# Kernel tuning notes

Hardware: AMD Instinct MI355X
Metric: run time of the kernel (lower is better)

The kernel has to match this reference:

```python
import jax, jax.numpy as jnp
import numpy as np

LN_EPS = 1e-5
LOCAL_SIZE = 256
N_HEAD, D_HEAD = 16, 64


def layer_norm_c(x):
    # layer norm over channel dim (axis=1), no affine params (matches F.layer_norm(x.T,(d,)).T)
    m = jnp.mean(x, axis=1, keepdims=True)
    v = jnp.var(x, axis=1, keepdims=True)
    return (x - m) / jnp.sqrt(v + LN_EPS)


def rel_shift(x):
    # x: [b, n, q, k] -> Transformer-XL relative shift
    b, n, q, k = x.shape
    x = jnp.pad(x, ((0, 0), (0, 0), (0, 0), (1, 0)))
    return x.reshape(b, n, k + 1, q)[:, :, 1:].reshape(b, n, q, k)


def setup_inputs() -> dict:
    key = jax.random.key(0)
    ks = jax.random.split(key, 14)
    bsz, d_model, qlen, mlen = 4, 1024, 512, 512
    klen = qlen + mlen
    d_inner = 4096
    s = lambda k, shape, sc=0.05: jax.random.normal(k, shape, dtype=jnp.float32) * sc
    return {
        "z1ss": jax.random.normal(ks[0], (bsz, d_model, qlen), dtype=jnp.float32),
        "uss": jax.random.normal(ks[1], (bsz, 3 * d_model, klen), dtype=jnp.float32) * 0.1,
        "z0": jax.random.normal(ks[2], (bsz, d_model, mlen), dtype=jnp.float32),
        "pos_emb": jax.random.normal(ks[3], (1, d_model, klen), dtype=jnp.float32),
        "qkv_w": s(ks[4], (3 * d_model, d_model)),
        "r_w": s(ks[5], (d_model, d_model)),
        "r_w_bias": s(ks[6], (N_HEAD, D_HEAD)),
        "r_r_bias": s(ks[7], (N_HEAD, D_HEAD)),
        "o_w": s(ks[8], (d_model, d_model)),
        "o_b": s(ks[9], (d_model,)),
        "ff1_w": s(ks[10], (d_inner, d_model)),
        "ff1_b": s(ks[11], (d_inner,)),
        "ff2_w": s(ks[12], (d_model, d_inner)),
        "ff2_b": s(ks[13], (d_model,)),
    }


def reference(z1ss, uss, z0, pos_emb, qkv_w, r_w, r_w_bias, r_r_bias, o_w, o_b,
              ff1_w, ff1_b, ff2_w, ff2_b):
    bsz, d_model, qlen = z1ss.shape
    mlen = z0.shape[2]
    n_head, d_head = N_HEAD, D_HEAD
    scale = 1.0 / d_head ** 0.5

    # ---- self-attention (post-lnorm path) ----
    cat = jnp.concatenate([z0, z1ss], axis=-1)              # [b, d, klen]
    klen = cat.shape[2]
    w_heads = jnp.einsum('od,bdk->bok', qkv_w, cat) + uss   # [b, 3d, klen]
    r_head_k = jnp.einsum('od,dk->ok', r_w, pos_emb[0])     # [d, rlen]
    rlen = r_head_k.shape[1]

    w_head_q, w_head_k, w_head_v = jnp.split(w_heads, 3, axis=1)
    w_head_q = w_head_q[:, :, -qlen:]
    w_head_q = w_head_q.reshape(bsz, n_head, d_head, qlen)
    w_head_k = w_head_k.reshape(bsz, n_head, d_head, klen)
    w_head_v = w_head_v.reshape(bsz, n_head, d_head, klen)
    r_head_k = r_head_k.reshape(n_head, d_head, rlen)

    rw_q = w_head_q + r_w_bias[:, :, None]                  # [b,n,d,q]
    AC = jnp.einsum('bndi,bndj->bnij', rw_q, w_head_k)      # [b,n,q,k]
    rr_q = w_head_q + r_r_bias[:, :, None]
    BD = rel_shift(jnp.einsum('bndi,ndj->bnij', rr_q, r_head_k))
    attn_score = (AC + BD) * scale

    local_size = LOCAL_SIZE if LOCAL_SIZE else 1000
    i = jnp.arange(qlen)[:, None]
    j = jnp.arange(klen)[None, :]
    mask = (j > i + mlen) | (j <= i + mlen - local_size)    # causal + local window
    attn_score = jnp.where(mask[None, None], -jnp.inf, attn_score)

    attn_prob = jax.nn.softmax(attn_score, axis=-1)
    attn_vec = jnp.einsum('bnij,bndj->bndi', attn_prob, w_head_v)
    attn_vec = attn_vec.reshape(bsz, n_head * d_head, qlen)
    attn_out = jnp.einsum('od,bdq->boq', o_w, attn_vec) + o_b[None, :, None]
    x = layer_norm_c(attn_out + z1ss)                       # post-lnorm

    # ---- position-wise FF (weight-shared, post-lnorm) ----
    h = jax.nn.relu(jnp.einsum('id,bdq->biq', ff1_w, x) + ff1_b[None, :, None])
    out2 = jnp.einsum('di,biq->bdq', ff2_w, h) + ff2_b[None, :, None]
    return layer_norm_c(out2 + x)
```

## Files before the change

kernel.cpp:

```cpp
#include <hip/hip_runtime.h>
#include <hip/hip_bf16.h>

typedef unsigned short u16;
typedef __attribute__((ext_vector_type(8))) short s8v;
typedef __attribute__((ext_vector_type(4))) short s4v;
typedef __attribute__((ext_vector_type(4))) float f4v;

__device__ __forceinline__ float s2f(u16 s) {
    unsigned int u = ((unsigned int)s) << 16;
    return __builtin_bit_cast(float, u);
}
__device__ __forceinline__ u16 f2s(float f) {
    __hip_bfloat16 h = __float2bfloat16(f);
    return __builtin_bit_cast(u16, h);
}

__device__ __forceinline__ void gl2lds16(const u16* g, u16* l) {
    __builtin_amdgcn_global_load_lds((const __attribute__((address_space(1))) void*)g,
                                     (__attribute__((address_space(3))) void*)l, 16, 0, 0);
}

#define BSZ 4
#define DM 1024
#define QLEN 512
#define MLEN 512
#define KLEN 1024
#define DI 4096
#define NH 16
#define DH 64
#define WIN 256

__global__ __launch_bounds__(256) void conv_w5(
    const float* __restrict__ s0, const float* __restrict__ s1,
    const float* __restrict__ s2, const float* __restrict__ s3,
    const float* __restrict__ s4,
    u16* __restrict__ d0, u16* __restrict__ d1, u16* __restrict__ d2,
    u16* __restrict__ d3, u16* __restrict__ d4)
{
    const int e0 = 786432, e1 = e0 + 262144, e2 = e1 + 262144,
              e3 = e2 + 1048576, e4 = e3 + 1048576;
    int i = blockIdx.x * 256 + threadIdx.x;
    const float* s; u16* d; int off;
    if (i < e0)      { s = s0; d = d0; off = i; }
    else if (i < e1) { s = s1; d = d1; off = i - e0; }
    else if (i < e2) { s = s2; d = d2; off = i - e1; }
    else if (i < e3) { s = s3; d = d3; off = i - e2; }
    else if (i < e4) { s = s4; d = d4; off = i - e3; }
    else return;
    f4v v = *(const f4v*)&s[(size_t)off * 4];
    s4v o;
#pragma unroll
    for (int k = 0; k < 4; ++k) o[k] = (short)f2s(v[k]);
    *(s4v*)&d[(size_t)off * 4] = o;
}

__global__ __launch_bounds__(256) void trans_f2b(
    const float* __restrict__ src, long sS, int ldS, int colOff,
    u16* __restrict__ dst, long sD, int ldD, int rowOff)
{
    __shared__ float tile[32][33];
    int b = blockIdx.z;
    int t0 = blockIdx.x * 32, f0 = blockIdx.y * 32;
    int tx = threadIdx.x, ty = threadIdx.y;
#pragma unroll
    for (int p = 0; p < 4; ++p)
        tile[ty + 8 * p][tx] = src[(size_t)b * sS + (size_t)(f0 + ty + 8 * p) * ldS + colOff + t0 + tx];
    __syncthreads();
#pragma unroll
    for (int p = 0; p < 4; ++p)
        dst[(size_t)b * sD + (size_t)(rowOff + t0 + ty + 8 * p) * ldD + f0 + tx] = f2s(tile[tx][ty + 8 * p]);
}

__global__ __launch_bounds__(256) void uss_add(
    const float* __restrict__ uss, u16* __restrict__ whT, u16* __restrict__ vT)
{
    __shared__ float tile[32][33];
    int b = blockIdx.z;
    int t0 = blockIdx.x * 32, fy = blockIdx.y;
    int tx = threadIdx.x, ty = threadIdx.y;
    if (fy < 32 && t0 < 512) return;
    const float* S = uss + (size_t)b * 3072 * 1024;
    if (fy < 64) {
        int f0 = fy * 32;
        u16* D = whT + (size_t)b * 1024 * 3072;
#pragma unroll
        for (int p = 0; p < 4; ++p)
            tile[ty + 8 * p][tx] = S[(size_t)(f0 + ty + 8 * p) * 1024 + t0 + tx];
        __syncthreads();
#pragma unroll
        for (int p = 0; p < 4; ++p) {
            size_t o = (size_t)(t0 + ty + 8 * p) * 3072 + f0 + tx;
            D[o] = f2s(s2f(D[o]) + tile[tx][ty + 8 * p]);
        }
    } else {
        int d0 = (fy - 64) * 32;
#pragma unroll
        for (int p = 0; p < 4; ++p) {
            int d = d0 + ty + 8 * p;
            size_t ui = ((size_t)2048 + d) * 1024 + t0 + tx;
            size_t vi = (size_t)d * 4096 + (size_t)b * KLEN + t0 + tx;
            vT[vi] = f2s(s2f(vT[vi]) + S[ui]);
        }
    }
}

__global__ __launch_bounds__(256) void trans_b2f(
    const u16* __restrict__ src, long sS, int ldS,
    float* __restrict__ dst, long sD, int ldD)
{
    __shared__ float tile[32][33];
    int b = blockIdx.z;
    int t0 = blockIdx.x * 32, f0 = blockIdx.y * 32;
    int tx = threadIdx.x, ty = threadIdx.y;
#pragma unroll
    for (int p = 0; p < 4; ++p)
        tile[ty + 8 * p][tx] = s2f(src[(size_t)b * sS + (size_t)(f0 + ty + 8 * p) * ldS + t0 + tx]);
    __syncthreads();
#pragma unroll
    for (int p = 0; p < 4; ++p)
        dst[(size_t)b * sD + (size_t)(t0 + ty + 8 * p) * ldD + f0 + tx] = tile[tx][ty + 8 * p];
}

template<int BN, int SPLIT>
__global__ __launch_bounds__(256) void gemm_bt(
    const u16* __restrict__ A,
    const u16* __restrict__ B,
    u16* __restrict__ C,
    float* __restrict__ fOut,
    int M, int K,
    const float* __restrict__ bias,
    int relu,
    int qskip,
    long pstride,
    u16* __restrict__ vTout)
{
    constexpr int BM = 128, BK = 64;
    constexpr int MI = (BN == 128) ? 4 : 2;
    constexpr int NI = 4;
    const int n0 = blockIdx.x * BN, m0 = blockIdx.y * BM;
    if (qskip && m0 + BM <= 1024 && (n0 & 1023) < 512) return;
    const int Ks = K / SPLIT;
    const int kbeg = blockIdx.z * Ks;
    __shared__ __align__(16) u16 As[BM * BK];
    __shared__ __align__(16) u16 Bs[BN * BK];
    const int tid = threadIdx.x, lane = tid & 63, wv = tid >> 6;
    const int l15 = lane & 15, quad = lane >> 4;
    const int wm = (BN == 128) ? (wv >> 1) * 64 : wv * 32;
    const int wn = (BN == 128) ? (wv & 1) * 64 : 0;
    f4v acc[MI][NI] = {};
    for (int kk = kbeg; kk < kbeg + Ks; kk += BK) {
        __syncthreads();
#pragma unroll
        for (int p = 0; p < (BM * 8) / 256; ++p) {
            int c = p * 256 + tid, r = c >> 3, q = c & 7, qs = q ^ (r & 7);
            gl2lds16(&A[(size_t)(m0 + r) * K + kk + qs * 8], &As[c * 8]);
        }
#pragma unroll
        for (int p = 0; p < (BN * 8) / 256; ++p) {
            int c = p * 256 + tid, r = c >> 3, q = c & 7, qs = q ^ (r & 7);
            gl2lds16(&B[(size_t)(n0 + r) * K + kk + qs * 8], &Bs[c * 8]);
        }
        __syncthreads();
#pragma unroll
        for (int k0 = 0; k0 < BK; k0 += 32) {
            s8v af[MI], bf[NI];
#pragma unroll
            for (int mi = 0; mi < MI; ++mi) {
                int r = wm + mi * 16 + l15;
                af[mi] = *(const s8v*)&As[r * BK + ((((k0 >> 3) + quad) ^ (r & 7)) << 3)];
            }
#pragma unroll
            for (int ni = 0; ni < NI; ++ni) {
                int r = wn + ni * 16 + l15;
                bf[ni] = *(const s8v*)&Bs[r * BK + ((((k0 >> 3) + quad) ^ (r & 7)) << 3)];
            }
#pragma unroll
            for (int mi = 0; mi < MI; ++mi)
#pragma unroll
                for (int ni = 0; ni < NI; ++ni)
                    acc[mi][ni] = __builtin_amdgcn_mfma_f32_16x16x32_bf16(af[mi], bf[ni], acc[mi][ni], 0, 0, 0);
        }
    }
    if (SPLIT > 1) {
        float* base = fOut + (long)blockIdx.z * pstride;
#pragma unroll
        for (int mi = 0; mi < MI; ++mi) {
            int m = m0 + wm + mi * 16 + quad * 4;
#pragma unroll
            for (int ni = 0; ni < NI; ++ni) {
                int n = n0 + wn + ni * 16 + l15;
                *(f4v*)&base[(size_t)n * M + m] = acc[mi][ni];
            }
        }
    } else if (vTout && m0 >= 2048) {
#pragma unroll
        for (int mi = 0; mi < MI; ++mi) {
            int m = m0 + wm + mi * 16 + quad * 4;
#pragma unroll
            for (int ni = 0; ni < NI; ++ni) {
                int n = n0 + wn + ni * 16 + l15;
#pragma unroll
                for (int r2 = 0; r2 < 4; ++r2)
                    vTout[(size_t)(m + r2 - 2048) * 4096 + n] = f2s(acc[mi][ni][r2]);
            }
        }
    } else {
#pragma unroll
        for (int mi = 0; mi < MI; ++mi) {
            int m = m0 + wm + mi * 16 + quad * 4;
            float bv[4] = {0.f, 0.f, 0.f, 0.f};
            if (bias) {
#pragma unroll
                for (int r2 = 0; r2 < 4; ++r2) bv[r2] = bias[m + r2];
            }
#pragma unroll
            for (int ni = 0; ni < NI; ++ni) {
                int n = n0 + wn + ni * 16 + l15;
                float o[4];
#pragma unroll
                for (int r2 = 0; r2 < 4; ++r2) o[r2] = acc[mi][ni][r2] + bv[r2];
                if (relu) {
#pragma unroll
                    for (int r2 = 0; r2 < 4; ++r2) o[r2] = fmaxf(o[r2], 0.f);
                }
                s4v st;
#pragma unroll
                for (int r2 = 0; r2 < 4; ++r2) st[r2] = (short)f2s(o[r2]);
                *(s4v*)&C[(size_t)n * M + m] = st;
            }
        }
    }
}

#define QT 32
#define SROW 260
__global__ __launch_bounds__(256, 4) void attn_mfma(
    const u16* __restrict__ WHT,
    const u16* __restrict__ VT,
    const u16* __restrict__ RT,
    const float* __restrict__ rwb, const float* __restrict__ rrb,
    u16* __restrict__ avT)
{
    __shared__ __align__(16) float sS[QT * SROW];

    const int qt = blockIdx.x, n = blockIdx.y, b = blockIdx.z;
    const int i0 = qt * QT, j0 = i0 + WIN + 1;
    const int tid = threadIdx.x, lane = tid & 63, wv = tid >> 6;
    const int l15 = lane & 15, quad = lane >> 4;
    const u16* W = WHT + (size_t)b * KLEN * (3 * DM);

    s8v qac[2][2], qbd[2][2];
#pragma unroll
    for (int h = 0; h < 2; ++h) {
        int qrow = MLEN + i0 + 16 * h + l15;
#pragma unroll
        for (int kc = 0; kc < 2; ++kc) {
            int col = n * DH + kc * 32 + quad * 8;
            s8v qv = *(const s8v*)&W[(size_t)qrow * (3 * DM) + col];
            s8v a, c;
#pragma unroll
            for (int e = 0; e < 8; ++e) {
                float qf = s2f((u16)qv[e]);
                a[e] = (short)f2s(qf + rwb[col + e]);
                c[e] = (short)f2s(qf + rrb[col + e]);
            }
            qac[h][kc] = a; qbd[h][kc] = c;
        }
    }

    for (int ci = wv; ci < 18; ci += 4) {
        int j = j0 + ci * 16 + l15; if (j > KLEN - 1) j = KLEN - 1;
        const u16* Kr = &W[(size_t)j * (3 * DM) + DM + n * DH + quad * 8];
        s8v k0 = *(const s8v*)Kr, k1 = *(const s8v*)(Kr + 32);
#pragma unroll
        for (int h = 0; h < 2; ++h) {
            f4v acc = {};
            acc = __builtin_amdgcn_mfma_f32_16x16x32_bf16(qac[h][0], k0, acc, 0, 0, 0);
            acc = __builtin_amdgcn_mfma_f32_16x16x32_bf16(qac[h][1], k1, acc, 0, 0, 0);
#pragma unroll
            for (int r2 = 0; r2 < 4; ++r2) {
                int qi = 16 * h + quad * 4 + r2;
                int t = ci * 16 + l15 - qi;
                if ((unsigned)t < 256u) sS[qi * SROW + t] = acc[r2];
            }
        }
    }
    __syncthreads();

#pragma unroll
    for (int cc = 0; cc < 4; ++cc) {
        int ci = wv + cc * 4;
        const u16* Rr = &RT[(size_t)(ci * 16 + l15) * DM + n * DH + quad * 8];
        s8v r0 = *(const s8v*)Rr, r1 = *(const s8v*)(Rr + 32);
#pragma unroll
        for (int h = 0; h < 2; ++h) {
            f4v acc = {};
            acc = __builtin_amdgcn_mfma_f32_16x16x32_bf16(qbd[h][0], r0, acc, 0, 0, 0);
            acc = __builtin_amdgcn_mfma_f32_16x16x32_bf16(qbd[h][1], r1, acc, 0, 0, 0);
#pragma unroll
            for (int r2 = 0; r2 < 4; ++r2) {
                int qi = 16 * h + quad * 4 + r2;
                sS[qi * SROW + ci * 16 + l15] += acc[r2];
            }
        }
    }
    __syncthreads();

    {
        int g = tid >> 4, l = tid & 15;
#pragma unroll
        for (int h = 0; h < 2; ++h) {
            int r = g + 16 * h;
            float vals[16], mx = -1e30f;
#pragma unroll
            for (int k = 0; k < 16; ++k) {
                float s = sS[r * SROW + l + 16 * k] * 0.125f;
                vals[k] = s; mx = fmaxf(mx, s);
            }
            asm volatile("" ::: "memory");
#pragma unroll
            for (int d = 1; d < 16; d <<= 1) mx = fmaxf(mx, __shfl_xor(mx, d, 16));
            float sum = 0.f;
#pragma unroll
            for (int k = 0; k < 16; ++k) { vals[k] = __expf(vals[k] - mx); sum += vals[k]; }
#pragma unroll
            for (int d = 1; d < 16; d <<= 1) sum += __shfl_xor(sum, d, 16);
            float inv = 1.f / sum;
            u16* sPr = (u16*)&sS[r * SROW];
#pragma unroll
            for (int k = 0; k < 16; ++k) sPr[r + 1 + l + 16 * k] = f2s(vals[k] * inv);
            if (l <= r) sPr[l] = 0;
            if (l + 16 <= r) sPr[l + 16] = 0;
            int p = r + 257 + l;
            if (p < 288) sPr[p] = 0;
            p += 16;
            if (p < 288) sPr[p] = 0;
        }
    }
    __syncthreads();

    const u16* sPu = (const u16*)sS;
    const size_t vbase = (size_t)(n * DH + wv * 16 + l15) * 4096
                       + (size_t)b * KLEN + (j0 - 1) + quad * 8;
    f4v o0 = {}, o1 = {};
#pragma unroll
    for (int kc = 0; kc < 9; ++kc) {
        s8v bb = *(const s8v*)&VT[vbase + kc * 32];
        s8v a0 = *(const s8v*)&sPu[(size_t)l15 * (2 * SROW) + kc * 32 + quad * 8];
        s8v a1 = *(const s8v*)&sPu[(size_t)(16 + l15) * (2 * SROW) + kc * 32 + quad * 8];
        o0 = __builtin_amdgcn_mfma_f32_16x16x32_bf16(a0, bb, o0, 0, 0, 0);
        o1 = __builtin_amdgcn_mfma_f32_16x16x32_bf16(a1, bb, o1, 0, 0, 0);
    }
#pragma unroll
    for (int r2 = 0; r2 < 4; ++r2) {
        int qi = quad * 4 + r2;
        avT[((size_t)b * QLEN + i0 + qi) * DM + n * DH + wv * 16 + l15] = f2s(o0[r2]);
        avT[((size_t)b * QLEN + i0 + 16 + qi) * DM + n * DH + wv * 16 + l15] = f2s(o1[r2]);
    }
}

__global__ __launch_bounds__(256) void ln_f(
    const float* __restrict__ P, long pstride, int nparts,
    const float* __restrict__ bias,
    const u16* __restrict__ res, int resMode, u16* __restrict__ out)
{
    int n = blockIdx.x, tid = threadIdx.x;
    int lane = tid & 63, wv = tid >> 6;
    int f = tid * 4;
    int rrow = resMode ? (((n >> 9) * 2 + 1) * 512 + (n & 511)) : n;
    f4v pv = *(const f4v*)&P[(size_t)n * DM + f];
    for (int p = 1; p < nparts; ++p) {
        const float* Pp = P + (long)p * pstride;
        pv += *(const f4v*)&Pp[(size_t)n * DM + f];
    }
    s4v rv = *(const s4v*)&res[(size_t)rrow * DM + f];
    f4v bv = *(const f4v*)&bias[f];
    float v[4];
#pragma unroll
    for (int k = 0; k < 4; ++k) v[k] = pv[k] + bv[k] + s2f((u16)rv[k]);
    float s = v[0] + v[1] + v[2] + v[3];
    float ss = v[0] * v[0] + v[1] * v[1] + v[2] * v[2] + v[3] * v[3];
#pragma unroll
    for (int d = 1; d < 64; d <<= 1) {
        s += __shfl_xor(s, d, 64);
        ss += __shfl_xor(ss, d, 64);
    }
    __shared__ float ps[4], pss[4];
    if (lane == 0) { ps[wv] = s; pss[wv] = ss; }
    __syncthreads();
    float S = ps[0] + ps[1] + ps[2] + ps[3];
    float SS = pss[0] + pss[1] + pss[2] + pss[3];
    float m = S * (1.f / DM);
    float var = SS * (1.f / DM) - m * m;
    float inv = rsqrtf(fmaxf(var, 0.f) + 1e-5f);
    s4v st;
#pragma unroll
    for (int k = 0; k < 4; ++k) st[k] = (short)f2s((v[k] - m) * inv);
    *(s4v*)&out[(size_t)n * DM + f] = st;
}

extern "C" void kernel_launch(void* const* d_in, const int* in_sizes, int n_in,
                              void* d_out, int out_size, void* d_ws, size_t ws_size,
                              hipStream_t stream) {
    const float* z1ss  = (const float*)d_in[0];
    const float* uss   = (const float*)d_in[1];
    const float* z0    = (const float*)d_in[2];
    const float* pos   = (const float*)d_in[3];
    const float* qkv_w = (const float*)d_in[4];
    const float* r_w   = (const float*)d_in[5];
    const float* rwb   = (const float*)d_in[6];
    const float* rrb   = (const float*)d_in[7];
    const float* o_w   = (const float*)d_in[8];
    const float* o_b   = (const float*)d_in[9];
    const float* ff1_w = (const float*)d_in[10];
    const float* ff1_b = (const float*)d_in[11];
    const float* ff2_w = (const float*)d_in[12];
    const float* ff2_b = (const float*)d_in[13];

    u16* ws = (u16*)d_ws;
    u16* wQ   = ws;
    u16* wR   = ws + 3145728;
    u16* wO   = ws + 4194304;
    u16* wF1  = ws + 5242880;
    u16* wF2  = ws + 9437184;
    u16* catT = ws + 13631488;
    u16* whT  = ws + 17825792;
    u16* posT = ws + 30408704;
    u16* rT   = ws + 30670848;
    u16* avT  = ws + 30932992;
    u16* xT   = ws + 33030144;
    float* pref = (float*)(ws + 35127296);
    u16* hT   = whT;
    u16* outT = catT;

    u16* vT = (u16*)pref;

    float* part1 = (float*)d_ws;
    long pstr = part1 - pref;

    dim3 tblk(32, 8);

    conv_w5<<<13312, 256, 0, stream>>>(qkv_w, r_w, o_w, ff1_w, ff2_w,
                                       wQ, wR, wO, wF1, wF2);

    trans_f2b<<<dim3(16, 32, BSZ), tblk, 0, stream>>>(z0, (long)DM * MLEN, MLEN, 0,
                                                      catT, (long)KLEN * DM, DM, 0);
    trans_f2b<<<dim3(16, 32, BSZ), tblk, 0, stream>>>(z1ss, (long)DM * QLEN, QLEN, 0,
                                                      catT, (long)KLEN * DM, DM, MLEN);
    trans_f2b<<<dim3(8, 32, 1), tblk, 0, stream>>>(pos, 0, KLEN, KLEN - WIN,
                                                   posT, 0, DM, 0);

    gemm_bt<64, 1><<<dim3(64, 24, 1), 256, 0, stream>>>(
        wQ, catT, whT, nullptr, 3 * DM, DM, nullptr, 0, 1, 0, vT);

    uss_add<<<dim3(32, 96, BSZ), tblk, 0, stream>>>(uss, whT, vT);

    gemm_bt<64, 1><<<dim3(4, 8, 1), 256, 0, stream>>>(
        wR, posT, rT, nullptr, DM, DM, nullptr, 0, 0, 0, nullptr);

    attn_mfma<<<dim3(QLEN / QT, NH, BSZ), 256, 0, stream>>>(whT, vT, rT, rwb, rrb, avT);

    gemm_bt<64, 2><<<dim3(32, 8, 2), 256, 0, stream>>>(
        wO, avT, nullptr, pref, DM, DM, nullptr, 0, 0, pstr, nullptr);

    ln_f<<<2048, 256, 0, stream>>>(pref, pstr, 2, o_b, catT, 1, xT);

    gemm_bt<64, 1><<<dim3(32, 32, 1), 256, 0, stream>>>(
        wF1, xT, hT, nullptr, DI, DM, ff1_b, 1, 0, 0, nullptr);

    gemm_bt<64, 2><<<dim3(32, 8, 2), 256, 0, stream>>>(
        wF2, hT, nullptr, pref, DM, DI, nullptr, 0, 0, pstr, nullptr);

    ln_f<<<2048, 256, 0, stream>>>(pref, pstr, 2, ff2_b, xT, 0, outT);

    trans_b2f<<<dim3(32, 16, BSZ), tblk, 0, stream>>>(outT, (long)QLEN * DM, DM,
                                                      (float*)d_out, (long)DM * QLEN, QLEN);
}
```

Measured before the change: 337.5 us.

## Merge prep kernels into one launch and double attention query tile to 64

Merges the weight conversion kernel and the three transpose kernels into a single prep launch, so three launches and their inter-kernel gaps go away. The attention kernel now handles 64 query rows per block instead of 32. Each K/R/V fragment load is reused across four 16-row MFMA groups, and the window overhead per query shrinks, in exchange for half as many blocks, a larger LDS score buffer and lower occupancy (launch bounds 2).

```diff
diff --git a/kernel.cpp b/kernel.cpp
--- a/kernel.cpp
+++ b/kernel.cpp
@@ -30,38 +30,56 @@
 #define DH 64
 #define WIN 256
 
-__global__ __launch_bounds__(256) void conv_w5(
-    const float* __restrict__ s0, const float* __restrict__ s1,
-    const float* __restrict__ s2, const float* __restrict__ s3,
-    const float* __restrict__ s4,
-    u16* __restrict__ d0, u16* __restrict__ d1, u16* __restrict__ d2,
-    u16* __restrict__ d3, u16* __restrict__ d4)
-{
-    const int e0 = 786432, e1 = e0 + 262144, e2 = e1 + 262144,
-              e3 = e2 + 1048576, e4 = e3 + 1048576;
-    int i = blockIdx.x * 256 + threadIdx.x;
-    const float* s; u16* d; int off;
-    if (i < e0)      { s = s0; d = d0; off = i; }
-    else if (i < e1) { s = s1; d = d1; off = i - e0; }
-    else if (i < e2) { s = s2; d = d2; off = i - e1; }
-    else if (i < e3) { s = s3; d = d3; off = i - e2; }
-    else if (i < e4) { s = s4; d = d4; off = i - e3; }
-    else return;
-    f4v v = *(const f4v*)&s[(size_t)off * 4];
-    s4v o;
-#pragma unroll
-    for (int k = 0; k < 4; ++k) o[k] = (short)f2s(v[k]);
-    *(s4v*)&d[(size_t)off * 4] = o;
-}
-
-__global__ __launch_bounds__(256) void trans_f2b(
-    const float* __restrict__ src, long sS, int ldS, int colOff,
-    u16* __restrict__ dst, long sD, int ldD, int rowOff)
-{
+#define CONV_BLKS 13312
+#define Z0_BLKS 2048
+#define Z1_BLKS 2048
+#define POS_BLKS 256
+__global__ __launch_bounds__(256) void prep(
+    const float* __restrict__ qkv_w, const float* __restrict__ r_w,
+    const float* __restrict__ o_w, const float* __restrict__ ff1_w,
+    const float* __restrict__ ff2_w,
+    u16* __restrict__ wQ, u16* __restrict__ wR, u16* __restrict__ wO,
+    u16* __restrict__ wF1, u16* __restrict__ wF2,
+    const float* __restrict__ z0, const float* __restrict__ z1ss,
+    const float* __restrict__ pos,
+    u16* __restrict__ catT, u16* __restrict__ posT)
+{
+    int bx = blockIdx.x, tid = threadIdx.x;
+    if (bx < CONV_BLKS) {
+        const int e0 = 786432, e1 = e0 + 262144, e2 = e1 + 262144, e3 = e2 + 1048576;
+        int i = bx * 256 + tid;
+        const float* s; u16* d; int off;
+        if (i < e0)      { s = qkv_w; d = wQ;  off = i; }
+        else if (i < e1) { s = r_w;   d = wR;  off = i - e0; }
+        else if (i < e2) { s = o_w;   d = wO;  off = i - e1; }
+        else if (i < e3) { s = ff1_w; d = wF1; off = i - e2; }
+        else             { s = ff2_w; d = wF2; off = i - e3; }
+        f4v v = *(const f4v*)&s[(size_t)off * 4];
+        s4v o;
+#pragma unroll
+        for (int k = 0; k < 4; ++k) o[k] = (short)f2s(v[k]);
+        *(s4v*)&d[(size_t)off * 4] = o;
+        return;
+    }
     __shared__ float tile[32][33];
-    int b = blockIdx.z;
-    int t0 = blockIdx.x * 32, f0 = blockIdx.y * 32;
-    int tx = threadIdx.x, ty = threadIdx.y;
+    int tx = tid & 31, ty = tid >> 5;
+    const float* src; u16* dst; long sS, sD; int ldS, ldD, colOff, rowOff, t0, f0, b;
+    if (bx < CONV_BLKS + Z0_BLKS) {
+        int idx = bx - CONV_BLKS;
+        t0 = (idx & 15) * 32; f0 = ((idx >> 4) & 31) * 32; b = idx >> 9;
+        src = z0;   sS = (long)DM * MLEN; ldS = MLEN; colOff = 0;
+        dst = catT; sD = (long)KLEN * DM; ldD = DM;  rowOff = 0;
+    } else if (bx < CONV_BLKS + Z0_BLKS + Z1_BLKS) {
+        int idx = bx - CONV_BLKS - Z0_BLKS;
+        t0 = (idx & 15) * 32; f0 = ((idx >> 4) & 31) * 32; b = idx >> 9;
+        src = z1ss; sS = (long)DM * QLEN; ldS = QLEN; colOff = 0;
+        dst = catT; sD = (long)KLEN * DM; ldD = DM;  rowOff = MLEN;
+    } else {
+        int idx = bx - CONV_BLKS - Z0_BLKS - Z1_BLKS;
+        t0 = (idx & 7) * 32; f0 = (idx >> 3) * 32; b = 0;
+        src = pos;  sS = 0; ldS = KLEN; colOff = KLEN - WIN;
+        dst = posT; sD = 0; ldD = DM;   rowOff = 0;
+    }
 #pragma unroll
     for (int p = 0; p < 4; ++p)
         tile[ty + 8 * p][tx] = src[(size_t)b * sS + (size_t)(f0 + ty + 8 * p) * ldS + colOff + t0 + tx];
@@ -232,9 +250,9 @@
     }
 }
 
-#define QT 32
+#define QT 64
 #define SROW 260
-__global__ __launch_bounds__(256, 4) void attn_mfma(
+__global__ __launch_bounds__(256, 2) void attn_mfma(
     const u16* __restrict__ WHT,
     const u16* __restrict__ VT,
     const u16* __restrict__ RT,
@@ -249,9 +267,9 @@
     const int l15 = lane & 15, quad = lane >> 4;
     const u16* W = WHT + (size_t)b * KLEN * (3 * DM);
 
-    s8v qac[2][2], qbd[2][2];
-#pragma unroll
-    for (int h = 0; h < 2; ++h) {
+    s8v qac[4][2], qbd[4][2];
+#pragma unroll
+    for (int h = 0; h < 4; ++h) {
         int qrow = MLEN + i0 + 16 * h + l15;
 #pragma unroll
         for (int kc = 0; kc < 2; ++kc) {
@@ -268,12 +286,12 @@
         }
     }
 
-    for (int ci = wv; ci < 18; ci += 4) {
+    for (int ci = wv; ci < 20; ci += 4) {
         int j = j0 + ci * 16 + l15; if (j > KLEN - 1) j = KLEN - 1;
         const u16* Kr = &W[(size_t)j * (3 * DM) + DM + n * DH + quad * 8];
         s8v k0 = *(const s8v*)Kr, k1 = *(const s8v*)(Kr + 32);
 #pragma unroll
-        for (int h = 0; h < 2; ++h) {
+        for (int h = 0; h < 4; ++h) {
             f4v acc = {};
             acc = __builtin_amdgcn_mfma_f32_16x16x32_bf16(qac[h][0], k0, acc, 0, 0, 0);
             acc = __builtin_amdgcn_mfma_f32_16x16x32_bf16(qac[h][1], k1, acc, 0, 0, 0);
@@ -293,7 +311,7 @@
         const u16* Rr = &RT[(size_t)(ci * 16 + l15) * DM + n * DH + quad * 8];
         s8v r0 = *(const s8v*)Rr, r1 = *(const s8v*)(Rr + 32);
 #pragma unroll
-        for (int h = 0; h < 2; ++h) {
+        for (int h = 0; h < 4; ++h) {
             f4v acc = {};
             acc = __builtin_amdgcn_mfma_f32_16x16x32_bf16(qbd[h][0], r0, acc, 0, 0, 0);
             acc = __builtin_amdgcn_mfma_f32_16x16x32_bf16(qbd[h][1], r1, acc, 0, 0, 0);
@@ -309,7 +327,7 @@
     {
         int g = tid >> 4, l = tid & 15;
 #pragma unroll
-        for (int h = 0; h < 2; ++h) {
+        for (int h = 0; h < 4; ++h) {
             int r = g + 16 * h;
             float vals[16], mx = -1e30f;
 #pragma unroll
@@ -329,12 +347,8 @@
             u16* sPr = (u16*)&sS[r * SROW];
 #pragma unroll
             for (int k = 0; k < 16; ++k) sPr[r + 1 + l + 16 * k] = f2s(vals[k] * inv);
-            if (l <= r) sPr[l] = 0;
-            if (l + 16 <= r) sPr[l + 16] = 0;
-            int p = r + 257 + l;
-            if (p < 288) sPr[p] = 0;
-            p += 16;
-            if (p < 288) sPr[p] = 0;
+            for (int p = l; p <= r; p += 16) sPr[p] = 0;
+            for (int p = r + 257 + l; p < 320; p += 16) sPr[p] = 0;
         }
     }
     __syncthreads();
@@ -342,21 +356,23 @@
     const u16* sPu = (const u16*)sS;
     const size_t vbase = (size_t)(n * DH + wv * 16 + l15) * 4096
                        + (size_t)b * KLEN + (j0 - 1) + quad * 8;
-    f4v o0 = {}, o1 = {};
-#pragma unroll
-    for (int kc = 0; kc < 9; ++kc) {
+    f4v o[4] = {};
+#pragma unroll
+    for (int kc = 0; kc < 10; ++kc) {
         s8v bb = *(const s8v*)&VT[vbase + kc * 32];
-        s8v a0 = *(const s8v*)&sPu[(size_t)l15 * (2 * SROW) + kc * 32 + quad * 8];
-        s8v a1 = *(const s8v*)&sPu[(size_t)(16 + l15) * (2 * SROW) + kc * 32 + quad * 8];
-        o0 = __builtin_amdgcn_mfma_f32_16x16x32_bf16(a0, bb, o0, 0, 0, 0);
-        o1 = __builtin_amdgcn_mfma_f32_16x16x32_bf16(a1, bb, o1, 0, 0, 0);
-    }
-#pragma unroll
-    for (int r2 = 0; r2 < 4; ++r2) {
-        int qi = quad * 4 + r2;
-        avT[((size_t)b * QLEN + i0 + qi) * DM + n * DH + wv * 16 + l15] = f2s(o0[r2]);
-        avT[((size_t)b * QLEN + i0 + 16 + qi) * DM + n * DH + wv * 16 + l15] = f2s(o1[r2]);
-    }
+#pragma unroll
+        for (int h = 0; h < 4; ++h) {
+            s8v a = *(const s8v*)&sPu[(size_t)(16 * h + l15) * (2 * SROW) + kc * 32 + quad * 8];
+            o[h] = __builtin_amdgcn_mfma_f32_16x16x32_bf16(a, bb, o[h], 0, 0, 0);
+        }
+    }
+#pragma unroll
+    for (int h = 0; h < 4; ++h)
+#pragma unroll
+        for (int r2 = 0; r2 < 4; ++r2) {
+            int qi = quad * 4 + r2;
+            avT[((size_t)b * QLEN + i0 + 16 * h + qi) * DM + n * DH + wv * 16 + l15] = f2s(o[h][r2]);
+        }
 }
 
 __global__ __launch_bounds__(256) void ln_f(
@@ -440,15 +456,9 @@
 
     dim3 tblk(32, 8);
 
-    conv_w5<<<13312, 256, 0, stream>>>(qkv_w, r_w, o_w, ff1_w, ff2_w,
-                                       wQ, wR, wO, wF1, wF2);
-
-    trans_f2b<<<dim3(16, 32, BSZ), tblk, 0, stream>>>(z0, (long)DM * MLEN, MLEN, 0,
-                                                      catT, (long)KLEN * DM, DM, 0);
-    trans_f2b<<<dim3(16, 32, BSZ), tblk, 0, stream>>>(z1ss, (long)DM * QLEN, QLEN, 0,
-                                                      catT, (long)KLEN * DM, DM, MLEN);
-    trans_f2b<<<dim3(8, 32, 1), tblk, 0, stream>>>(pos, 0, KLEN, KLEN - WIN,
-                                                   posT, 0, DM, 0);
+    prep<<<CONV_BLKS + Z0_BLKS + Z1_BLKS + POS_BLKS, 256, 0, stream>>>(
+        qkv_w, r_w, o_w, ff1_w, ff2_w, wQ, wR, wO, wF1, wF2,
+        z0, z1ss, pos, catT, posT);
 
     gemm_bt<64, 1><<<dim3(64, 24, 1), 256, 0, stream>>>(
         wQ, catT, whT, nullptr, 3 * DM, DM, nullptr, 0, 1, 0, vT);
```

New measurement: 325.9 us. 3.4% less time.
